# Optimization experiments

Measured on AMD Instinct MI355X. Metric: run time of the kernel, lower is better.

The kernel has to match this reference:

```python
import jax, jax.numpy as jnp
import numpy as np

B, N, E, HID, ED, NH = 2, 10000, 160000, 128, 32, 8
HD = HID // NH  # head_dim = 16
EPS = 1e-5


def setup_inputs() -> dict:
    key = jax.random.key(0)
    ks = jax.random.split(key, 12)
    s = 0.05  # keep pre-tanh activations in a sane range
    return {
        "h": jax.random.normal(ks[0], (B, N, HID), jnp.float32),
        "edge_attr": jax.random.normal(ks[1], (B, E, ED), jnp.float32),
        "edge_index": jax.random.randint(ks[2], (E, 2), 0, N),
        "Wq": jax.random.normal(ks[3], (HID, HID), jnp.float32) * s,
        "bq": jnp.zeros((HID,), jnp.float32),
        "Wk": jax.random.normal(ks[4], (HID, HID), jnp.float32) * s,
        "bk": jnp.zeros((HID,), jnp.float32),
        "Wv": jax.random.normal(ks[5], (HID, HID), jnp.float32) * s,
        "bv": jnp.zeros((HID,), jnp.float32),
        "We": jax.random.normal(ks[6], (HID, ED), jnp.float32) * s,
        "be": jnp.zeros((HID,), jnp.float32),
        "attn_vec": jax.random.normal(ks[7], (NH, HD), jnp.float32) * 0.02,
        "Ws": jax.random.normal(ks[8], (HID, HID), jnp.float32) * s,
        "bs": jnp.zeros((HID,), jnp.float32),
        "Wa": jax.random.normal(ks[9], (HID, HID), jnp.float32) * s,
        "ba": jnp.zeros((HID,), jnp.float32),
        "ln_g": jnp.ones((HID,), jnp.float32),
        "ln_b": jnp.zeros((HID,), jnp.float32),
    }


def reference(h, edge_attr, edge_index, Wq, bq, Wk, bk, Wv, bv, We, be,
              attn_vec, Ws, bs, Wa, ba, ln_g, ln_b):
    src = edge_index[:, 0]
    dst = edge_index[:, 1]
    b, n, hid = h.shape
    e_cnt = src.shape[0]

    h_src = h[:, src, :]  # [B,E,HID]
    h_dst = h[:, dst, :]

    q = (h_dst @ Wq.T + bq).reshape(b, e_cnt, NH, HD)
    k = (h_src @ Wk.T + bk).reshape(b, e_cnt, NH, HD)
    v = (h_src @ Wv.T + bv).reshape(b, e_cnt, NH, HD)
    e = (edge_attr @ We.T + be).reshape(b, e_cnt, NH, HD)

    # GATv2-style scores: [B,E,NH]
    logits = jnp.einsum('behd,hd->beh', jnp.tanh(q + k + e), attn_vec)
    logits = logits / np.float32(np.sqrt(HD))

    # segment softmax over edges grouped by dst node (stable)
    lt = jnp.transpose(logits, (1, 0, 2))  # [E,B,NH]
    mx = jax.ops.segment_max(lt, dst, num_segments=n)  # [N,B,NH]
    ex = jnp.exp(lt - mx[dst])
    den = jax.ops.segment_sum(ex, dst, num_segments=n)
    alpha = jnp.transpose(ex / den[dst], (1, 0, 2))  # [B,E,NH]

    msg = (alpha[..., None] * (v + e)).reshape(b, e_cnt, hid)  # [B,E,HID]
    agg = jax.ops.segment_sum(jnp.transpose(msg, (1, 0, 2)), dst, num_segments=n)
    agg = jnp.transpose(agg, (1, 0, 2))  # [B,N,HID]

    update = (h @ Ws.T + bs) + (agg @ Wa.T + ba)
    x = h + jax.nn.gelu(update, approximate=False)  # dropout is identity in eval

    mu = jnp.mean(x, axis=-1, keepdims=True)
    var = jnp.var(x, axis=-1, keepdims=True)
    return (x - mu) / jnp.sqrt(var + EPS) * ln_g + ln_b
```

## Files before the change

kernel.cpp:

```cpp
#include <hip/hip_runtime.h>
#include <math.h>
#include <stdint.h>

#define B_   2
#define N_   10000
#define E_   160000
#define HID_ 128
#define ED_  32
#define NH_  8
#define HD_  16
#define ROWS_ (B_ * N_)

using half2_t = __attribute__((ext_vector_type(2))) _Float16;
using f16x8   = __attribute__((ext_vector_type(8))) _Float16;
using f32x4   = __attribute__((ext_vector_type(4))) float;

__device__ __forceinline__ half2_t f2h2(float a, float b) {
    return __builtin_bit_cast(half2_t, __builtin_amdgcn_cvt_pkrtz(a, b));
}
__device__ __forceinline__ uint32_t pkh2(float a, float b) {
    return __builtin_bit_cast(uint32_t, __builtin_amdgcn_cvt_pkrtz(a, b));
}
__device__ __forceinline__ uint16_t f2h(float v) {
    return __builtin_bit_cast(uint16_t, (_Float16)v);
}


__global__ void hist_kernel(const int* __restrict__ ei, int* __restrict__ deg, int E) {
    int e = blockIdx.x * 256 + threadIdx.x;
    if (e < E) atomicAdd(&deg[ei[2 * e + 1]], 1);
}

__global__ __launch_bounds__(256) void scan_kernel(const int* __restrict__ deg,
                                                   int* __restrict__ off, int N) {
    __shared__ int sums[256];
    int t = threadIdx.x;
    int chunk = (N + 255) / 256;
    int s0 = t * chunk, s1 = min(N, s0 + chunk);
    int s = 0;
    for (int i = s0; i < s1; ++i) s += deg[i];
    sums[t] = s;
    __syncthreads();
    #pragma unroll
    for (int d = 1; d < 256; d <<= 1) {
        int v = (t >= d) ? sums[t - d] : 0;
        __syncthreads();
        sums[t] += v;
        __syncthreads();
    }
    if (t == 255) off[N] = sums[255];
    int run = sums[t] - s;
    for (int i = s0; i < s1; ++i) { off[i] = run; run += deg[i]; }
}

__global__ void fill_kernel(const int* __restrict__ ei, const int* __restrict__ off,
                            int* __restrict__ cursor, int* __restrict__ csr,
                            int* __restrict__ srcs, int E) {
    int e = blockIdx.x * 256 + threadIdx.x;
    if (e < E) {
        int2 se = *(const int2*)(ei + 2 * e);
        int p = atomicAdd(&cursor[se.y], 1);
        int o = off[se.y] + p;
        csr[o] = e;
        srcs[o] = se.x;
    }
}


#define GM 64
#define LDA 68

__global__ __launch_bounds__(256) void qkvs_kernel(
    const float* __restrict__ h,
    const float* __restrict__ Wq, const float* __restrict__ bq,
    const float* __restrict__ Wk, const float* __restrict__ bk,
    const float* __restrict__ Wv, const float* __restrict__ bv,
    const float* __restrict__ Ws, const float* __restrict__ bs,
    const float* __restrict__ ba,
    float* __restrict__ Q, uint16_t* __restrict__ Kv16, float* __restrict__ S)
{
    __shared__ uint32_t As[GM * LDA];
    __shared__ uint32_t Bs[128 * LDA];
    __shared__ float bsm[512];

    int tid = threadIdx.x;
    int lane = tid & 63;
    int wave = tid >> 6;
    int row0 = blockIdx.x * GM;

    for (int f = tid; f < 512; f += 256) {
        float v;
        if (f < 128)      v = bq[f];
        else if (f < 256) v = bk[f - 128];
        else if (f < 384) v = bv[f - 256];
        else              v = bs[f - 384] + ba[f - 384];
        bsm[f] = v;
    }

    for (int f = tid; f < GM * 32; f += 256) {
        int r = f >> 5, c4 = f & 31;
        long row = row0 + r;
        float4 hv = (row < ROWS_) ? *(const float4*)(h + row * HID_ + c4 * 4)
                                  : make_float4(0.f, 0.f, 0.f, 0.f);
        As[r * LDA + c4 * 2]     = pkh2(hv.x, hv.y);
        As[r * LDA + c4 * 2 + 1] = pkh2(hv.z, hv.w);
    }

    int lq = lane & 15;
    int ar = wave * 16 + lq;

    for (int jc = 0; jc < 4; ++jc) {
        int J0 = jc * 128;
        __syncthreads();
        for (int f = tid; f < 128 * 32; f += 256) {
            int jr = f >> 5, c4 = f & 31;
            int J = J0 + jr;
            const float* Wp;
            if (J < 128)      Wp = Wq + (long)J * HID_;
            else if (J < 256) Wp = Wk + (long)(J - 128) * HID_;
            else if (J < 384) Wp = Wv + (long)(J - 256) * HID_;
            else              Wp = Ws + (long)(J - 384) * HID_;
            float4 wv = *(const float4*)(Wp + c4 * 4);
            Bs[jr * LDA + c4 * 2]     = pkh2(wv.x, wv.y);
            Bs[jr * LDA + c4 * 2 + 1] = pkh2(wv.z, wv.w);
        }
        __syncthreads();

        f32x4 acc[8];
        #pragma unroll
        for (int nt = 0; nt < 8; ++nt) {
            float c = bsm[J0 + nt * 16 + lq];
            acc[nt] = (f32x4){ c, c, c, c };
        }

        #pragma unroll
        for (int ks = 0; ks < 4; ++ks) {
            f16x8 a = *(const f16x8*)(As + ar * LDA + ks * 16 + (lane >> 4) * 4);
            #pragma unroll
            for (int nt = 0; nt < 8; ++nt) {
                f16x8 b = *(const f16x8*)(Bs + (nt * 16 + lq) * LDA + ks * 16 + (lane >> 4) * 4);
                acc[nt] = __builtin_amdgcn_mfma_f32_16x16x32_f16(a, b, acc[nt], 0, 0, 0);
            }
        }

        #pragma unroll
        for (int nt = 0; nt < 8; ++nt) {
            int J = J0 + nt * 16 + lq;
            long rbase = row0 + wave * 16 + (lane >> 4) * 4;
            #pragma unroll
            for (int r = 0; r < 4; ++r) {
                long row = rbase + r;
                if (row < ROWS_) {
                    float v = acc[nt][r];
                    if (J < 128)      Q[row * 128 + J] = v;
                    else if (J < 256) Kv16[row * 256 + 2 * (J - 128)] = f2h(v);
                    else if (J < 384) Kv16[row * 256 + 2 * (J - 256) + 1] = f2h(v);
                    else              S[row * 128 + (J - 384)] = v;
                }
            }
        }
    }
}


template <int CTRL>
__device__ __forceinline__ float dpp_add(float x) {
    int y = __builtin_amdgcn_mov_dpp(__float_as_int(x), CTRL, 0xF, 0xF, true);
    return x + __int_as_float(y);
}
__device__ __forceinline__ float hsum16(float p) {
    p = dpp_add<0xB1>(p);
    p = dpp_add<0x4E>(p);
    p = dpp_add<0x141>(p);
    p = dpp_add<0x140>(p);
    return p;
}


#define NPB 4
#define CHUNK 96
#define EAS 20

__global__ __launch_bounds__(128) void node_kernel(
    const float* __restrict__ edge_attr,
    const float* __restrict__ Q, const uint32_t* __restrict__ KVp,
    const float* __restrict__ We, const float* __restrict__ be,
    const float* __restrict__ attn_vec,
    const int* __restrict__ off, const int* __restrict__ csr,
    const int* __restrict__ srcs,
    uint16_t* __restrict__ aggh)
{
    int n0 = blockIdx.x * NPB;
    int b  = blockIdx.y;
    int j  = threadIdx.x;
    long bN = (long)b * N_;

    __shared__ int sL[CHUNK];
    __shared__ uint32_t eaL[CHUNK * EAS];

    half2_t we16[16];
    {
        const float4* We4 = (const float4*)(We + (long)j * ED_);
        #pragma unroll
        for (int c = 0; c < 8; ++c) {
            float4 w = We4[c];
            we16[2 * c]     = f2h2(w.x, w.y);
            we16[2 * c + 1] = f2h2(w.z, w.w);
        }
    }
    float bej = be[j];
    float avj = attn_vec[j] * 0.25f;

    float q0 = Q[(bN + n0 + 0) * 128 + j];
    float q1 = Q[(bN + n0 + 1) * 128 + j];
    float q2 = Q[(bN + n0 + 2) * 128 + j];
    float q3 = Q[(bN + n0 + 3) * 128 + j];

    int o0 = off[n0];
    int c1 = off[n0 + 1] - o0, c2 = off[n0 + 2] - o0,
        c3 = off[n0 + 3] - o0, c4_ = off[n0 + 4] - o0;
    int total = c4_;

    const float* eab = edge_attr + (long)b * E_ * ED_;
    const uint32_t* KVb = KVp + bN * 128;

    float acc0 = 0.f, den0 = 0.f, acc1 = 0.f, den1 = 0.f;
    float acc2 = 0.f, den2 = 0.f, acc3 = 0.f, den3 = 0.f;

    auto edge_body = [&](int i, float qg, float& accg, float& deng) {
        int s = sL[i];
        half2_t kv = __builtin_bit_cast(half2_t, KVb[(long)s * 128 + j]);
        float eja = bej, ejb = 0.f;
        const half2_t* ea = (const half2_t*)(eaL + i * EAS);
        #pragma unroll
        for (int c = 0; c < 8; ++c) {
            eja = __builtin_amdgcn_fdot2(we16[c], ea[c], eja, false);
            ejb = __builtin_amdgcn_fdot2(we16[c + 8], ea[c + 8], ejb, false);
        }
        float ej = eja + ejb;
        float y = qg + (float)kv.x + ej;
        float t = 1.f - 2.f * __builtin_amdgcn_rcpf(__expf(2.f * y) + 1.f);
        float p = hsum16(t * avj);
        float ex = __expf(p);
        deng += ex;
        accg += ex * ((float)kv.y + ej);
    };

    auto range_loop = [&](int lo, int hi, float qg, float& accg, float& deng) {
        int i = lo;
        for (; i + 3 < hi; i += 4) {
            edge_body(i, qg, accg, deng);
            edge_body(i + 1, qg, accg, deng);
            edge_body(i + 2, qg, accg, deng);
            edge_body(i + 3, qg, accg, deng);
        }
        for (; i < hi; ++i) edge_body(i, qg, accg, deng);
    };

    for (int tau = 0; tau < total; tau += CHUNK) {
        int rows = min(total - tau, CHUNK);
        __syncthreads();
        for (int t = j; t < rows; t += 128)
            sL[t] = srcs[o0 + tau + t];
        for (int idx = j; idx < rows * 8; idx += 128) {
            int r = idx >> 3, c = idx & 7;
            int e = csr[o0 + tau + r];
            float4 f = *(const float4*)(eab + (long)e * ED_ + c * 4);
            eaL[r * EAS + 2 * c]     = pkh2(f.x, f.y);
            eaL[r * EAS + 2 * c + 1] = pkh2(f.z, f.w);
        }
        __syncthreads();

        range_loop(max(0 - tau, 0),   min(c1 - tau, rows), q0, acc0, den0);
        range_loop(max(c1 - tau, 0),  min(c2 - tau, rows), q1, acc1, den1);
        range_loop(max(c2 - tau, 0),  min(c3 - tau, rows), q2, acc2, den2);
        range_loop(max(c3 - tau, 0),  min(c4_ - tau, rows), q3, acc3, den3);
    }

    aggh[(bN + n0 + 0) * 128 + j] = f2h((c1 > 0)   ? acc0 * __builtin_amdgcn_rcpf(den0) : 0.f);
    aggh[(bN + n0 + 1) * 128 + j] = f2h((c2 > c1)  ? acc1 * __builtin_amdgcn_rcpf(den1) : 0.f);
    aggh[(bN + n0 + 2) * 128 + j] = f2h((c3 > c2)  ? acc2 * __builtin_amdgcn_rcpf(den2) : 0.f);
    aggh[(bN + n0 + 3) * 128 + j] = f2h((c4_ > c3) ? acc3 * __builtin_amdgcn_rcpf(den3) : 0.f);
}


__global__ __launch_bounds__(256) void wa_ln_kernel(
    const uint16_t* __restrict__ aggh,
    const float* __restrict__ Wa,
    const float* __restrict__ S, const float* __restrict__ h,
    const float* __restrict__ ln_g, const float* __restrict__ ln_b,
    float* __restrict__ out)
{
    __shared__ uint32_t As[GM * LDA];
    __shared__ uint32_t Bs[128 * LDA];

    int tid = threadIdx.x;
    int lane = tid & 63;
    int wave = tid >> 6;
    int row0 = blockIdx.x * GM;

    const uint32_t* Xa = (const uint32_t*)aggh;
    for (int f = tid; f < GM * 16; f += 256) {
        int r = f >> 4, c = f & 15;
        long row = row0 + r;
        uint4 v = (row < ROWS_) ? *(const uint4*)(Xa + row * 64 + c * 4)
                                : make_uint4(0u, 0u, 0u, 0u);
        *(uint4*)(&As[r * LDA + c * 4]) = v;
    }
    for (int f = tid; f < 128 * 32; f += 256) {
        int jr = f >> 5, c4 = f & 31;
        float4 wv = *(const float4*)(Wa + (long)jr * HID_ + c4 * 4);
        Bs[jr * LDA + c4 * 2]     = pkh2(wv.x, wv.y);
        Bs[jr * LDA + c4 * 2 + 1] = pkh2(wv.z, wv.w);
    }
    __syncthreads();

    f32x4 acc[8];
    #pragma unroll
    for (int nt = 0; nt < 8; ++nt) acc[nt] = (f32x4){ 0.f, 0.f, 0.f, 0.f };

    int lq = lane & 15;
    int ar = wave * 16 + lq;
    #pragma unroll
    for (int ks = 0; ks < 4; ++ks) {
        f16x8 a = *(const f16x8*)(As + ar * LDA + ks * 16 + (lane >> 4) * 4);
        #pragma unroll
        for (int nt = 0; nt < 8; ++nt) {
            f16x8 b = *(const f16x8*)(Bs + (nt * 16 + lq) * LDA + ks * 16 + (lane >> 4) * 4);
            acc[nt] = __builtin_amdgcn_mfma_f32_16x16x32_f16(a, b, acc[nt], 0, 0, 0);
        }
    }

    float gJ[8], bJ[8];
    #pragma unroll
    for (int nt = 0; nt < 8; ++nt) {
        int J = nt * 16 + lq;
        gJ[nt] = ln_g[J];
        bJ[nt] = ln_b[J];
    }
    long rbase = row0 + wave * 16 + (lane >> 4) * 4;
    #pragma unroll
    for (int r = 0; r < 4; ++r) {
        long row = rbase + r;
        if (row < ROWS_) {
            float xv[8];
            float sum = 0.f, sum2 = 0.f;
            #pragma unroll
            for (int nt = 0; nt < 8; ++nt) {
                int J = nt * 16 + lq;
                float upd = acc[nt][r] + S[row * 128 + J];
                float ge = 0.5f * upd * (1.f + erff(upd * 0.70710678118654752f));
                float x = h[row * 128 + J] + ge;
                xv[nt] = x;
                sum += x;
                sum2 += x * x;
            }
            sum = hsum16(sum);
            sum2 = hsum16(sum2);
            float mu = sum * (1.f / 128.f);
            float var = sum2 * (1.f / 128.f) - mu * mu;
            float rs = rsqrtf(var + 1e-5f);
            #pragma unroll
            for (int nt = 0; nt < 8; ++nt)
                out[row * 128 + nt * 16 + lq] = (xv[nt] - mu) * rs * gJ[nt] + bJ[nt];
        }
    }
}


extern "C" void kernel_launch(void* const* d_in, const int* in_sizes, int n_in,
                              void* d_out, int out_size, void* d_ws, size_t ws_size,
                              hipStream_t stream) {
    const float* h         = (const float*)d_in[0];
    const float* edge_attr = (const float*)d_in[1];
    const int*   ei        = (const int*)  d_in[2];
    const float* Wq = (const float*)d_in[3];
    const float* bq = (const float*)d_in[4];
    const float* Wk = (const float*)d_in[5];
    const float* bk = (const float*)d_in[6];
    const float* Wv = (const float*)d_in[7];
    const float* bv = (const float*)d_in[8];
    const float* We = (const float*)d_in[9];
    const float* be = (const float*)d_in[10];
    const float* attn_vec = (const float*)d_in[11];
    const float* Ws = (const float*)d_in[12];
    const float* bs = (const float*)d_in[13];
    const float* Wa = (const float*)d_in[14];
    const float* ba = (const float*)d_in[15];
    const float* ln_g = (const float*)d_in[16];
    const float* ln_b = (const float*)d_in[17];
    float* out = (float*)d_out;

    size_t p = 0;
    auto alloc = [&](size_t bytes) { size_t r = p; p += (bytes + 255) & ~(size_t)255; return r; };
    char* ws = (char*)d_ws;
    float*    Q    = (float*)(ws + alloc((size_t)ROWS_ * 128 * 4));
    uint16_t* Kv16 = (uint16_t*)(ws + alloc((size_t)ROWS_ * 256 * 2));
    float*    S    = (float*)(ws + alloc((size_t)ROWS_ * 128 * 4));
    uint16_t* aggh = (uint16_t*)(ws + alloc((size_t)ROWS_ * 128 * 2));
    int* dc     = (int*)(ws + alloc((size_t)2 * N_ * 4));
    int* off    = (int*)(ws + alloc((size_t)(N_ + 1) * 4));
    int* csr    = (int*)(ws + alloc((size_t)E_ * 4));
    int* srcs   = (int*)(ws + alloc((size_t)E_ * 4));
    int* deg = dc;
    int* cursor = dc + N_;
    (void)ws_size;

    hipMemsetAsync(dc, 0, (size_t)2 * N_ * 4, stream);
    hist_kernel<<<(E_ + 255) / 256, 256, 0, stream>>>(ei, deg, E_);
    scan_kernel<<<1, 256, 0, stream>>>(deg, off, N_);
    fill_kernel<<<(E_ + 255) / 256, 256, 0, stream>>>(ei, off, cursor, csr, srcs, E_);

    qkvs_kernel<<<(ROWS_ + GM - 1) / GM, 256, 0, stream>>>(h, Wq, bq, Wk, bk, Wv, bv,
                                                           Ws, bs, ba, Q, Kv16, S);

    dim3 grid(N_ / NPB, B_);
    node_kernel<<<grid, 128, 0, stream>>>(edge_attr, Q, (const uint32_t*)Kv16,
                                          We, be, attn_vec, off, csr, srcs, aggh);

    wa_ln_kernel<<<(ROWS_ + GM - 1) / GM, 256, 0, stream>>>(aggh, Wa, S, h,
                                                            ln_g, ln_b, out);
}
```

Measured before the change: 180.9 us.

## Remap node kernel to one wavefront with two channels per thread

The node aggregation kernel now runs one 64-thread wavefront per block over two nodes. Each thread handles two adjacent hidden channels, so a head spans 8 lanes and the score reduction needs one fewer DPP step. Because the block is a single wave, the __syncthreads calls around the shared edge-attribute staging are dropped. K/V and Q are loaded as 8-byte vectors and the output is written as packed halves. The trade-off is more registers per thread for two We rows, and correctness now depends on implicit intra-wave ordering of LDS accesses.

```diff
diff --git a/kernel.cpp b/kernel.cpp
--- a/kernel.cpp
+++ b/kernel.cpp
@@ -168,6 +168,12 @@
     int y = __builtin_amdgcn_mov_dpp(__float_as_int(x), CTRL, 0xF, 0xF, true);
     return x + __int_as_float(y);
 }
+__device__ __forceinline__ float hsum8(float p) {
+    p = dpp_add<0xB1>(p);
+    p = dpp_add<0x4E>(p);
+    p = dpp_add<0x141>(p);
+    return p;
+}
 __device__ __forceinline__ float hsum16(float p) {
     p = dpp_add<0xB1>(p);
     p = dpp_add<0x4E>(p);
@@ -177,11 +183,11 @@
 }
 
 
-#define NPB 4
-#define CHUNK 96
-#define EAS 20
-
-__global__ __launch_bounds__(128) void node_kernel(
+#define NPB 2
+#define CHUNK 64
+#define EAS 18
+
+__global__ __launch_bounds__(64, 4) void node_kernel(
     const float* __restrict__ edge_attr,
     const float* __restrict__ Q, const uint32_t* __restrict__ KVp,
     const float* __restrict__ We, const float* __restrict__ be,
@@ -192,95 +198,105 @@
 {
     int n0 = blockIdx.x * NPB;
     int b  = blockIdx.y;
-    int j  = threadIdx.x;
+    int t  = threadIdx.x;
     long bN = (long)b * N_;
 
     __shared__ int sL[CHUNK];
     __shared__ uint32_t eaL[CHUNK * EAS];
 
-    half2_t we16[16];
+    half2_t we0[16], we1[16];
     {
-        const float4* We4 = (const float4*)(We + (long)j * ED_);
+        const float4* W0 = (const float4*)(We + (long)(2 * t) * ED_);
+        const float4* W1 = (const float4*)(We + (long)(2 * t + 1) * ED_);
         #pragma unroll
         for (int c = 0; c < 8; ++c) {
-            float4 w = We4[c];
-            we16[2 * c]     = f2h2(w.x, w.y);
-            we16[2 * c + 1] = f2h2(w.z, w.w);
-        }
-    }
-    float bej = be[j];
-    float avj = attn_vec[j] * 0.25f;
-
-    float q0 = Q[(bN + n0 + 0) * 128 + j];
-    float q1 = Q[(bN + n0 + 1) * 128 + j];
-    float q2 = Q[(bN + n0 + 2) * 128 + j];
-    float q3 = Q[(bN + n0 + 3) * 128 + j];
+            float4 w = W0[c];
+            we0[2 * c]     = f2h2(w.x, w.y);
+            we0[2 * c + 1] = f2h2(w.z, w.w);
+            float4 v = W1[c];
+            we1[2 * c]     = f2h2(v.x, v.y);
+            we1[2 * c + 1] = f2h2(v.z, v.w);
+        }
+    }
+    float2 bev = *(const float2*)(be + 2 * t);
+    float2 av  = *(const float2*)(attn_vec + 2 * t);
+    av.x *= 0.25f; av.y *= 0.25f;
+
+    float2 q0 = *(const float2*)(Q + (bN + n0 + 0) * 128 + 2 * t);
+    float2 q1 = *(const float2*)(Q + (bN + n0 + 1) * 128 + 2 * t);
 
     int o0 = off[n0];
-    int c1 = off[n0 + 1] - o0, c2 = off[n0 + 2] - o0,
-        c3 = off[n0 + 3] - o0, c4_ = off[n0 + 4] - o0;
-    int total = c4_;
+    int c1 = off[n0 + 1] - o0, c2 = off[n0 + 2] - o0;
+    int total = c2;
 
     const float* eab = edge_attr + (long)b * E_ * ED_;
     const uint32_t* KVb = KVp + bN * 128;
 
-    float acc0 = 0.f, den0 = 0.f, acc1 = 0.f, den1 = 0.f;
-    float acc2 = 0.f, den2 = 0.f, acc3 = 0.f, den3 = 0.f;
-
-    auto edge_body = [&](int i, float qg, float& accg, float& deng) {
+    float a00 = 0.f, a01 = 0.f, den0 = 0.f;
+    float a10 = 0.f, a11 = 0.f, den1 = 0.f;
+
+    auto edge_body = [&](int i, const float2& qg, float& af0, float& af1, float& deng) {
         int s = sL[i];
-        half2_t kv = __builtin_bit_cast(half2_t, KVb[(long)s * 128 + j]);
-        float eja = bej, ejb = 0.f;
+        uint2 kvu = *(const uint2*)(KVb + (long)s * 128 + 2 * t);
+        half2_t kv0 = __builtin_bit_cast(half2_t, kvu.x);
+        half2_t kv1 = __builtin_bit_cast(half2_t, kvu.y);
         const half2_t* ea = (const half2_t*)(eaL + i * EAS);
+        float e0a = bev.x, e0b = 0.f, e1a = bev.y, e1b = 0.f;
         #pragma unroll
         for (int c = 0; c < 8; ++c) {
-            eja = __builtin_amdgcn_fdot2(we16[c], ea[c], eja, false);
-            ejb = __builtin_amdgcn_fdot2(we16[c + 8], ea[c + 8], ejb, false);
-        }
-        float ej = eja + ejb;
-        float y = qg + (float)kv.x + ej;
-        float t = 1.f - 2.f * __builtin_amdgcn_rcpf(__expf(2.f * y) + 1.f);
-        float p = hsum16(t * avj);
+            half2_t eac = ea[c], ead = ea[c + 8];
+            e0a = __builtin_amdgcn_fdot2(we0[c], eac, e0a, false);
+            e0b = __builtin_amdgcn_fdot2(we0[c + 8], ead, e0b, false);
+            e1a = __builtin_amdgcn_fdot2(we1[c], eac, e1a, false);
+            e1b = __builtin_amdgcn_fdot2(we1[c + 8], ead, e1b, false);
+        }
+        float ej0 = e0a + e0b;
+        float ej1 = e1a + e1b;
+        float y0 = qg.x + (float)kv0.x + ej0;
+        float y1 = qg.y + (float)kv1.x + ej1;
+        float t0 = 1.f - 2.f * __builtin_amdgcn_rcpf(__expf(2.f * y0) + 1.f);
+        float t1 = 1.f - 2.f * __builtin_amdgcn_rcpf(__expf(2.f * y1) + 1.f);
+        float p = hsum8(t0 * av.x + t1 * av.y);
         float ex = __expf(p);
         deng += ex;
-        accg += ex * ((float)kv.y + ej);
+        af0 += ex * ((float)kv0.y + ej0);
+        af1 += ex * ((float)kv1.y + ej1);
     };
 
-    auto range_loop = [&](int lo, int hi, float qg, float& accg, float& deng) {
+    auto range_loop = [&](int lo, int hi, const float2& qg,
+                          float& af0, float& af1, float& deng) {
         int i = lo;
         for (; i + 3 < hi; i += 4) {
-            edge_body(i, qg, accg, deng);
-            edge_body(i + 1, qg, accg, deng);
-            edge_body(i + 2, qg, accg, deng);
-            edge_body(i + 3, qg, accg, deng);
-        }
-        for (; i < hi; ++i) edge_body(i, qg, accg, deng);
+            edge_body(i, qg, af0, af1, deng);
+            edge_body(i + 1, qg, af0, af1, deng);
+            edge_body(i + 2, qg, af0, af1, deng);
+            edge_body(i + 3, qg, af0, af1, deng);
+        }
+        for (; i < hi; ++i) edge_body(i, qg, af0, af1, deng);
     };
 
     for (int tau = 0; tau < total; tau += CHUNK) {
         int rows = min(total - tau, CHUNK);
-        __syncthreads();
-        for (int t = j; t < rows; t += 128)
-            sL[t] = srcs[o0 + tau + t];
-        for (int idx = j; idx < rows * 8; idx += 128) {
+        if (t < rows) sL[t] = srcs[o0 + tau + t];
+        for (int idx = t; idx < rows * 8; idx += 64) {
             int r = idx >> 3, c = idx & 7;
             int e = csr[o0 + tau + r];
             float4 f = *(const float4*)(eab + (long)e * ED_ + c * 4);
             eaL[r * EAS + 2 * c]     = pkh2(f.x, f.y);
             eaL[r * EAS + 2 * c + 1] = pkh2(f.z, f.w);
         }
-        __syncthreads();
-
-        range_loop(max(0 - tau, 0),   min(c1 - tau, rows), q0, acc0, den0);
-        range_loop(max(c1 - tau, 0),  min(c2 - tau, rows), q1, acc1, den1);
-        range_loop(max(c2 - tau, 0),  min(c3 - tau, rows), q2, acc2, den2);
-        range_loop(max(c3 - tau, 0),  min(c4_ - tau, rows), q3, acc3, den3);
-    }
-
-    aggh[(bN + n0 + 0) * 128 + j] = f2h((c1 > 0)   ? acc0 * __builtin_amdgcn_rcpf(den0) : 0.f);
-    aggh[(bN + n0 + 1) * 128 + j] = f2h((c2 > c1)  ? acc1 * __builtin_amdgcn_rcpf(den1) : 0.f);
-    aggh[(bN + n0 + 2) * 128 + j] = f2h((c3 > c2)  ? acc2 * __builtin_amdgcn_rcpf(den2) : 0.f);
-    aggh[(bN + n0 + 3) * 128 + j] = f2h((c4_ > c3) ? acc3 * __builtin_amdgcn_rcpf(den3) : 0.f);
+
+        range_loop(max(0 - tau, 0),  min(c1 - tau, rows), q0, a00, a01, den0);
+        range_loop(max(c1 - tau, 0), min(c2 - tau, rows), q1, a10, a11, den1);
+    }
+
+    uint32_t* aggp = (uint32_t*)aggh;
+    {
+        float r0 = (c1 > 0) ? __builtin_amdgcn_rcpf(den0) : 0.f;
+        float r1 = (c2 > c1) ? __builtin_amdgcn_rcpf(den1) : 0.f;
+        aggp[(bN + n0 + 0) * 64 + t] = pkh2(a00 * r0, a01 * r0);
+        aggp[(bN + n0 + 1) * 64 + t] = pkh2(a10 * r1, a11 * r1);
+    }
 }
 
 
@@ -415,8 +431,8 @@
                                                            Ws, bs, ba, Q, Kv16, S);
 
     dim3 grid(N_ / NPB, B_);
-    node_kernel<<<grid, 128, 0, stream>>>(edge_attr, Q, (const uint32_t*)Kv16,
-                                          We, be, attn_vec, off, csr, srcs, aggh);
+    node_kernel<<<grid, 64, 0, stream>>>(edge_attr, Q, (const uint32_t*)Kv16,
+                                         We, be, attn_vec, off, csr, srcs, aggh);
 
     wa_ln_kernel<<<(ROWS_ + GM - 1) / GM, 256, 0, stream>>>(aggh, Wa, S, h,
                                                             ln_g, ln_b, out);
```

Result: no change. 183.7 us (+1.5%).
